# Kernel optimization log

Measured on AMD Instinct MI355X. Metric: run time of the kernel, lower is better.

Reference implementation:

```python
import jax, jax.numpy as jnp
import numpy as np

EMBED_DIM = 1024
NUM_HEADS = 16
HEAD_DIM = EMBED_DIM // NUM_HEADS


def setup_inputs() -> dict:
    key = jax.random.key(0)
    ks = jax.random.split(key, 9)
    B, N, D = 2, 2048, EMBED_DIM
    s = 1.0 / np.sqrt(D)
    inp = {
        "x": jax.random.normal(ks[0], (B, N, D), dtype=jnp.float32),
        "Wq": jax.random.uniform(ks[1], (D, D), jnp.float32, -s, s),
        "bq": jnp.zeros((D,), jnp.float32),
        "Wk": jax.random.uniform(ks[2], (D, D), jnp.float32, -s, s),
        "bk": jnp.zeros((D,), jnp.float32),
        "Wv": jax.random.uniform(ks[3], (D, D), jnp.float32, -s, s),
        "bv": jnp.zeros((D,), jnp.float32),
        "Wo": jax.random.uniform(ks[4], (D, D), jnp.float32, -s, s),
        "bo": jnp.zeros((D,), jnp.float32),
        "is_causal": 0,
    }
    return inp


def reference(x, Wq, bq, Wk, bk, Wv, bv, Wo, bo, is_causal):
    B, N, D = x.shape
    H, Hd = NUM_HEADS, HEAD_DIM
    # projections -> (B, H, N, Hd)
    def proj(W, b):
        return (x @ W.T + b).reshape(B, N, H, Hd).transpose(0, 2, 1, 3)
    q = proj(Wq, bq)
    k = proj(Wk, bk)
    v = proj(Wv, bv)
    # scaled dot-product attention with full (B,H,N,N) scores
    dots = jnp.einsum("bhqd,bhkd->bhqk", q, k) / np.sqrt(Hd).astype(np.float32)
    if is_causal:
        mask = jnp.tril(jnp.ones((N, N), dtype=bool))
        dots = jnp.where(mask, dots, -jnp.inf)
    attn = jax.nn.softmax(dots, axis=-1)
    out = jnp.einsum("bhqk,bhkd->bhqd", attn, v)  # (B,H,N,Hd)
    out = out.transpose(0, 2, 1, 3).reshape(B, N, D)
    return out @ Wo.T + bo
```

## Files before the change

### kernel.cpp

```cpp
#include <hip/hip_runtime.h>
#include <hip/hip_bf16.h>
#include <cstdint>
#include <cstddef>

#define DEVI __device__ __forceinline__

typedef __attribute__((ext_vector_type(8))) __bf16 bf16x8;
typedef __attribute__((ext_vector_type(4))) float  f32x4;
typedef __attribute__((ext_vector_type(4))) unsigned int uint4v;
typedef __attribute__((ext_vector_type(2))) unsigned int uint2v;

static constexpr int D_EMB = 1024;
static constexpr int NH    = 16;
static constexpr int HDIM  = 64;
static constexpr int BATCH = 2;
static constexpr int SEQ   = 2048;
static constexpr int MTOK  = BATCH * SEQ;
static constexpr int NQKV  = 3 * D_EMB;
static constexpr float L2E = 1.44269504088896340736f;
static constexpr float CSCALE = 0.125f * L2E;

#if __has_builtin(__builtin_amdgcn_exp2f)
#define EXP2F(x) __builtin_amdgcn_exp2f(x)
#else
#define EXP2F(x) exp2f(x)
#endif

typedef __attribute__((address_space(1))) unsigned int* gas_u32;
typedef __attribute__((address_space(3))) unsigned int* las_u32;

DEVI void gl_lds16(const void* g, void* l) {
  __builtin_amdgcn_global_load_lds((gas_u32)(void*)g, (las_u32)l, 16, 0, 0);
}

DEVI unsigned pack2bf(float lo, float hi) {
  unsigned short a = __builtin_bit_cast(unsigned short, (__bf16)lo);
  unsigned short b = __builtin_bit_cast(unsigned short, (__bf16)hi);
  return (unsigned)a | ((unsigned)b << 16);
}

__global__ __launch_bounds__(256) void cast_kernel(const float* __restrict__ in,
                                                   __bf16* __restrict__ out, int n8) {
  int i = blockIdx.x * 256 + threadIdx.x;
  if (i >= n8) return;
  const f32x4* p = (const f32x4*)(in + (size_t)i * 8);
  f32x4 a = p[0], b = p[1];
  bf16x8 o;
  o[0] = (__bf16)a[0]; o[1] = (__bf16)a[1]; o[2] = (__bf16)a[2]; o[3] = (__bf16)a[3];
  o[4] = (__bf16)b[0]; o[5] = (__bf16)b[1]; o[6] = (__bf16)b[2]; o[7] = (__bf16)b[3];
  *(bf16x8*)(out + (size_t)i * 8) = o;
}

__global__ __launch_bounds__(256) void cast_w4(const float* __restrict__ Wq,
                                               const float* __restrict__ Wk,
                                               const float* __restrict__ Wv,
                                               const float* __restrict__ Wo,
                                               __bf16* __restrict__ Wcat,
                                               __bf16* __restrict__ Wob) {
  const int which = blockIdx.y;
  const float* src = which == 0 ? Wq : which == 1 ? Wk : which == 2 ? Wv : Wo;
  __bf16* dst = which < 3 ? Wcat + (size_t)which * D_EMB * D_EMB : Wob;
  int i = blockIdx.x * 256 + threadIdx.x;
  const f32x4* p = (const f32x4*)(src + (size_t)i * 8);
  f32x4 a = p[0], b = p[1];
  bf16x8 o;
  o[0] = (__bf16)a[0]; o[1] = (__bf16)a[1]; o[2] = (__bf16)a[2]; o[3] = (__bf16)a[3];
  o[4] = (__bf16)b[0]; o[5] = (__bf16)b[1]; o[6] = (__bf16)b[2]; o[7] = (__bf16)b[3];
  *(bf16x8*)(dst + (size_t)i * 8) = o;
}

__global__ __launch_bounds__(512, 1) void gemm_qkv(const __bf16* __restrict__ A,
                                                   const __bf16* __restrict__ Bw,
                                                   const float* __restrict__ b0,
                                                   const float* __restrict__ b1,
                                                   const float* __restrict__ b2,
                                                   __bf16* __restrict__ C,
                                                   __bf16* __restrict__ Vt) {
  constexpr int lda = D_EMB, ldb = D_EMB, ldc = NQKV;
  constexpr int NT = D_EMB / 64;
  __shared__ __align__(16) unsigned char lds[131072];
  const int t = threadIdx.x;
  const int lane = t & 63, w = t >> 6;
  const int c = lane & 15, g = lane >> 4;
  const int wr = w >> 2, wc = w & 3;

  int fid = blockIdx.y * 12 + blockIdx.x;
  fid = (fid & 7) * 24 + (fid >> 3);
  const int bx = fid % 12, by = fid / 12;
  const int brow = by * 256, bcol = bx * 256;

  f32x4 acc[8][4] = {};

  int srow[2], schk[2];
#pragma unroll
  for (int i = 0; i < 2; i++) {
    int lb = i * 8192 + t * 16;
    int row = lb >> 7, ch = (lb & 127) >> 4;
    srow[i] = row; schk[i] = ch ^ (row & 7);
  }

  int offk[2];
#pragma unroll
  for (int kk = 0; kk < 2; kk++) offk[kk] = (((kk * 4 + g) ^ (c & 7)) << 4);
  int rowA[8], rowB[4];
#pragma unroll
  for (int m = 0; m < 8; m++) rowA[m] = (wr * 128 + m * 16 + c) * 128;
#pragma unroll
  for (int n = 0; n < 4; n++) rowB[n] = (wc * 64 + n * 16 + c) * 128;

#define STG_HALF(p, TN, NOFS)                                                       \
  do {                                                                              \
    if ((p) < 2) {                                                                  \
      _Pragma("unroll")                                                             \
      for (int i = 0; i < 2; i++)                                                   \
        gl_lds16(A + (size_t)(brow + (p) * 128 + srow[i]) * lda + (TN) * 64 + schk[i] * 8, \
                 lds + (NOFS) + (p) * 16384 + i * 8192 + t * 16);                   \
    } else {                                                                        \
      _Pragma("unroll")                                                             \
      for (int i = 0; i < 2; i++)                                                   \
        gl_lds16(Bw + (size_t)(bcol + ((p) & 1) * 128 + srow[i]) * ldb + (TN) * 64 + schk[i] * 8, \
                 lds + (NOFS) + 32768 + ((p) & 1) * 16384 + i * 8192 + t * 16);     \
    }                                                                               \
  } while (0)

#define PHASE(p, BOFS, NOFS, TN1, DO_STG)                                           \
  do {                                                                              \
    bf16x8 af[2][2];                                                                \
    if ((p) == 0) {                                                                 \
      _Pragma("unroll")                                                             \
      for (int n = 0; n < 4; n++)                                                   \
        _Pragma("unroll")                                                           \
        for (int kk = 0; kk < 2; kk++)                                              \
          bfr[n][kk] = *(const bf16x8*)(lds + (BOFS) + 32768 + rowB[n] + offk[kk]); \
    }                                                                               \
    _Pragma("unroll")                                                               \
    for (int mm = 0; mm < 2; mm++)                                                  \
      _Pragma("unroll")                                                             \
      for (int kk = 0; kk < 2; kk++)                                                \
        af[mm][kk] = *(const bf16x8*)(lds + (BOFS) + rowA[(p) * 2 + mm] + offk[kk]); \
    if (DO_STG) STG_HALF(p, TN1, NOFS);                                             \
    __builtin_amdgcn_s_barrier();                                                   \
    __builtin_amdgcn_s_setprio(1);                                                  \
    _Pragma("unroll")                                                               \
    for (int mm = 0; mm < 2; mm++)                                                  \
      _Pragma("unroll")                                                             \
      for (int n = 0; n < 4; n++)                                                   \
        _Pragma("unroll")                                                           \
        for (int kk = 0; kk < 2; kk++)                                              \
          acc[(p) * 2 + mm][n] = __builtin_amdgcn_mfma_f32_16x16x32_bf16(           \
              af[mm][kk], bfr[n][kk], acc[(p) * 2 + mm][n], 0, 0, 0);               \
    __builtin_amdgcn_s_setprio(0);                                                  \
    if ((p) == 3) asm volatile("s_waitcnt vmcnt(0)" ::: "memory");                  \
    __builtin_amdgcn_s_barrier();                                                   \
  } while (0)

#pragma unroll
  for (int p = 0; p < 4; p++) STG_HALF(p, 0, 0);
  __syncthreads();

  for (int tt = 0; tt < NT; tt += 2) {
    {
      bf16x8 bfr[4][2];
      const bool ds = (tt + 1 < NT);
      PHASE(0, 0, 65536, tt + 1, ds);
      PHASE(1, 0, 65536, tt + 1, ds);
      PHASE(2, 0, 65536, tt + 1, ds);
      PHASE(3, 0, 65536, tt + 1, ds);
    }
    {
      bf16x8 bfr[4][2];
      const bool ds = (tt + 2 < NT);
      PHASE(0, 65536, 0, tt + 2, ds);
      PHASE(1, 65536, 0, tt + 2, ds);
      PHASE(2, 65536, 0, tt + 2, ds);
      PHASE(3, 65536, 0, tt + 2, ds);
    }
  }
#undef STG_HALF
#undef PHASE

#pragma unroll
  for (int n = 0; n < 4; n++) {
    int col = bcol + wc * 64 + n * 16 + c;
    const float* bp = col < 1024 ? b0 : (col < 2048 ? b1 : b2);
    float bv = bp[col & 1023];
    float sc = col < 1024 ? CSCALE : 1.0f;
#pragma unroll
    for (int m = 0; m < 8; m++) {
      int row0 = brow + wr * 128 + m * 16 + g * 4;
      float v0 = (acc[m][n][0] + bv) * sc;
      float v1 = (acc[m][n][1] + bv) * sc;
      float v2 = (acc[m][n][2] + bv) * sc;
      float v3 = (acc[m][n][3] + bv) * sc;
      if (col >= 2048) {
        int cv = col - 2048;
        int h = cv >> 6, d = cv & 63;
        int bq = row0 >> 11;
        size_t vaddr = ((size_t)((bq * NH + h) * HDIM + d)) * SEQ + (row0 & (SEQ - 1));
        uint2v uu;
        uu[0] = pack2bf(v0, v1);
        uu[1] = pack2bf(v2, v3);
        *(uint2v*)(Vt + vaddr) = uu;
      } else {
        C[(size_t)(row0 + 0) * ldc + col] = (__bf16)v0;
        C[(size_t)(row0 + 1) * ldc + col] = (__bf16)v1;
        C[(size_t)(row0 + 2) * ldc + col] = (__bf16)v2;
        C[(size_t)(row0 + 3) * ldc + col] = (__bf16)v3;
      }
    }
  }
}

template <typename OutT, int BM>
__global__ __launch_bounds__(256) void gemm_bt(const __bf16* __restrict__ A,
                                               const __bf16* __restrict__ B,
                                               const float* __restrict__ b0,
                                               OutT* __restrict__ C,
                                               int K, int lda, int ldb, int ldc) {
  constexpr int ACH = BM / 32;
  constexpr int MR  = BM / 32;
  __shared__ __align__(16) unsigned char lds[BM * 128 + 16384];
  unsigned char* As = lds;
  unsigned char* Bs = lds + BM * 128;
  const int t = threadIdx.x;
  const int lane = t & 63;
  const int w = t >> 6;
  const int c = lane & 15, g = lane >> 4;
  const int wr = w >> 1, wc = w & 1;
  const int brow = blockIdx.y * BM;
  const int bcol = blockIdx.x * 128;

  f32x4 acc[MR][4] = {};

  int rs[4], chs[4];
#pragma unroll
  for (int i = 0; i < 4; i++) {
    int lb = i * 4096 + t * 16;
    int row = lb >> 7, ch = (lb & 127) >> 4;
    rs[i] = row; chs[i] = ch ^ (row & 7);
  }

  for (int k0 = 0; k0 < K; k0 += 64) {
#pragma unroll
    for (int i = 0; i < ACH; i++)
      gl_lds16(A + (size_t)(brow + rs[i]) * lda + k0 + chs[i] * 8,
               As + i * 4096 + t * 16);
#pragma unroll
    for (int i = 0; i < 4; i++)
      gl_lds16(B + (size_t)(bcol + rs[i]) * ldb + k0 + chs[i] * 8,
               Bs + i * 4096 + t * 16);
    __syncthreads();
#pragma unroll
    for (int kk = 0; kk < 2; kk++) {
      bf16x8 af[MR], bfr[4];
#pragma unroll
      for (int m = 0; m < MR; m++) {
        int row = wr * (BM / 2) + m * 16 + c;
        int ch = (kk * 4 + g) ^ (row & 7);
        af[m] = *(const bf16x8*)(As + row * 128 + ch * 16);
      }
#pragma unroll
      for (int n = 0; n < 4; n++) {
        int row = wc * 64 + n * 16 + c;
        int ch = (kk * 4 + g) ^ (row & 7);
        bfr[n] = *(const bf16x8*)(Bs + row * 128 + ch * 16);
      }
      __builtin_amdgcn_s_setprio(1);
#pragma unroll
      for (int m = 0; m < MR; m++)
#pragma unroll
        for (int n = 0; n < 4; n++)
          acc[m][n] = __builtin_amdgcn_mfma_f32_16x16x32_bf16(af[m], bfr[n], acc[m][n], 0, 0, 0);
      __builtin_amdgcn_s_setprio(0);
    }
    __syncthreads();
  }

#pragma unroll
  for (int n = 0; n < 4; n++) {
    int col = bcol + wc * 64 + n * 16 + c;
    float bv = b0[col];
#pragma unroll
    for (int m = 0; m < MR; m++) {
      int row0 = brow + wr * (BM / 2) + m * 16 + g * 4;
#pragma unroll
      for (int r = 0; r < 4; r++) {
        float v = acc[m][n][r] + bv;
        C[(size_t)(row0 + r) * ldc + col] = (OutT)v;
      }
    }
  }
}

__global__ __launch_bounds__(256, 2) void attn_fwd(const __bf16* __restrict__ Q,
                                                   const __bf16* __restrict__ Kg,
                                                   const __bf16* __restrict__ Vt,
                                                   __bf16* __restrict__ AO,
                                                   const int* __restrict__ causal_p) {
  __shared__ __align__(16) unsigned char lds[65536];
  const int t = threadIdx.x;
  const int lane = t & 63;
  const int w = t >> 6;
  const int c = lane & 15, g = lane >> 4;
  const int qhalf = w >> 1, parity = w & 1;
  const int bh = blockIdx.y;
  const int b = bh >> 4, h = bh & 15;
  const int q0 = blockIdx.x * 128;
  const int causal = causal_p[0];
  const int qbase = q0 + qhalf * 64;

  bf16x8 qf[4][2];
#pragma unroll
  for (int u = 0; u < 4; u++)
#pragma unroll
    for (int kk = 0; kk < 2; kk++)
      qf[u][kk] = *(const bf16x8*)(Q + (size_t)(b * SEQ + qbase + u * 16 + c) * NQKV +
                                   h * HDIM + kk * 32 + g * 8);

  f32x4 oacc[4][4] = {};
  float lrun[4] = {0.f, 0.f, 0.f, 0.f};

  int srow[2], schk[2];
#pragma unroll
  for (int i = 0; i < 2; i++) {
    int lb = i * 4096 + t * 16;
    int row = lb >> 7, ch = (lb & 127) >> 4;
    int sig = (row & 3) | ((row & 8) >> 1);
    srow[i] = row; schk[i] = ch ^ sig;
  }

  int voffK[8], voffV[8];
#pragma unroll
  for (int n = 0; n < 4; n++) {
    int row = ((n >> 1) << 5) + ((c >> 2) << 3) + ((n & 1) << 2) + (c & 3);
    int sig = (row & 3) | ((row & 8) >> 1);
#pragma unroll
    for (int kk = 0; kk < 2; kk++)
      voffK[n * 2 + kk] = parity * 16384 + row * 128 + (((kk * 4 + g) ^ sig) << 4);
  }
#pragma unroll
  for (int dt = 0; dt < 4; dt++) {
    int row = dt * 16 + c;
    int sig = (row & 3) | ((row & 8) >> 1);
#pragma unroll
    for (int kk2 = 0; kk2 < 2; kk2++)
      voffV[dt * 2 + kk2] = parity * 16384 + 8192 + row * 128 + (((kk2 * 4 + g) ^ sig) << 4);
  }

  const __bf16* Kbase = Kg + (size_t)b * SEQ * NQKV + h * HDIM;
  const __bf16* Vbase = Vt + (size_t)bh * HDIM * SEQ;

  const int kvend = causal ? (q0 + 128 < SEQ ? q0 + 128 : SEQ) : SEQ;
  const int npair = kvend >> 7;

#define STAGE_PAIR(JP, PB)                                                          \
  do {                                                                              \
    int kvn = (JP) << 7;                                                            \
    _Pragma("unroll")                                                               \
    for (int i = 0; i < 2; i++) {                                                   \
      gl_lds16(Kbase + (size_t)(kvn + srow[i]) * NQKV + schk[i] * 8,                \
               lds + (PB) + i * 4096 + t * 16);                                     \
      gl_lds16(Vbase + (size_t)srow[i] * SEQ + kvn + schk[i] * 8,                   \
               lds + (PB) + 8192 + i * 4096 + t * 16);                              \
      gl_lds16(Kbase + (size_t)(kvn + 64 + srow[i]) * NQKV + schk[i] * 8,           \
               lds + (PB) + 16384 + i * 4096 + t * 16);                             \
      gl_lds16(Vbase + (size_t)srow[i] * SEQ + kvn + 64 + schk[i] * 8,              \
               lds + (PB) + 24576 + i * 4096 + t * 16);                             \
    }                                                                               \
  } while (0)

#define ATTN_STEP(JV, BOFS, PBNEXT)                                                 \
  do {                                                                              \
    if ((JV) + 1 < npair) STAGE_PAIR((JV) + 1, PBNEXT);                             \
    f32x4 st[4][4] = {};                                                            \
    __builtin_amdgcn_s_setprio(1);                                                  \
    _Pragma("unroll")                                                               \
    for (int n = 0; n < 4; n++) {                                                   \
      _Pragma("unroll")                                                             \
      for (int kk = 0; kk < 2; kk++) {                                              \
        bf16x8 kf = *(const bf16x8*)(lds + (BOFS) + voffK[n * 2 + kk]);             \
        st[0][n] = __builtin_amdgcn_mfma_f32_16x16x32_bf16(kf, qf[0][kk], st[0][n], 0, 0, 0); \
        st[1][n] = __builtin_amdgcn_mfma_f32_16x16x32_bf16(kf, qf[1][kk], st[1][n], 0, 0, 0); \
        st[2][n] = __builtin_amdgcn_mfma_f32_16x16x32_bf16(kf, qf[2][kk], st[2][n], 0, 0, 0); \
        st[3][n] = __builtin_amdgcn_mfma_f32_16x16x32_bf16(kf, qf[3][kk], st[3][n], 0, 0, 0); \
      }                                                                             \
    }                                                                               \
    __builtin_amdgcn_s_setprio(0);                                                  \
    if (causal) {                                                                   \
      const int kv0 = ((JV) << 7) + parity * 64;                                    \
      _Pragma("unroll")                                                             \
      for (int u = 0; u < 4; u++) {                                                 \
        const int qrow_u = qbase + u * 16 + c;                                      \
        _Pragma("unroll")                                                           \
        for (int n = 0; n < 4; n++) {                                               \
          _Pragma("unroll")                                                         \
          for (int r = 0; r < 4; r++) {                                             \
            int kabs = kv0 + ((n >> 1) << 5) + (g << 3) + ((n & 1) << 2) + r;       \
            if (kabs > qrow_u) st[u][n][r] = -3.0e38f;                              \
          }                                                                         \
        }                                                                           \
      }                                                                             \
    }                                                                               \
    bf16x8 pfrag[4][2];                                                             \
    _Pragma("unroll")                                                               \
    for (int u = 0; u < 4; u++) {                                                   \
      _Pragma("unroll")                                                             \
      for (int n = 0; n < 4; n++) {                                                 \
        st[u][n][0] = EXP2F(st[u][n][0]);                                           \
        st[u][n][1] = EXP2F(st[u][n][1]);                                           \
        st[u][n][2] = EXP2F(st[u][n][2]);                                           \
        st[u][n][3] = EXP2F(st[u][n][3]);                                           \
      }                                                                             \
      float ps0 = (st[u][0][0] + st[u][0][1]) + (st[u][0][2] + st[u][0][3]);        \
      float ps1 = (st[u][1][0] + st[u][1][1]) + (st[u][1][2] + st[u][1][3]);        \
      float ps2 = (st[u][2][0] + st[u][2][1]) + (st[u][2][2] + st[u][2][3]);        \
      float ps3 = (st[u][3][0] + st[u][3][1]) + (st[u][3][2] + st[u][3][3]);        \
      lrun[u] += (ps0 + ps1) + (ps2 + ps3);                                         \
      _Pragma("unroll")                                                             \
      for (int kk2 = 0; kk2 < 2; kk2++) {                                           \
        int n0i = 2 * kk2, n1i = 2 * kk2 + 1;                                       \
        uint4v uu;                                                                  \
        uu[0] = pack2bf(st[u][n0i][0], st[u][n0i][1]);                              \
        uu[1] = pack2bf(st[u][n0i][2], st[u][n0i][3]);                              \
        uu[2] = pack2bf(st[u][n1i][0], st[u][n1i][1]);                              \
        uu[3] = pack2bf(st[u][n1i][2], st[u][n1i][3]);                              \
        pfrag[u][kk2] = __builtin_bit_cast(bf16x8, uu);                             \
      }                                                                             \
    }                                                                               \
    __builtin_amdgcn_s_setprio(1);                                                  \
    _Pragma("unroll")                                                               \
    for (int dt = 0; dt < 4; dt++) {                                                \
      _Pragma("unroll")                                                             \
      for (int kk2 = 0; kk2 < 2; kk2++) {                                           \
        bf16x8 vf = *(const bf16x8*)(lds + (BOFS) + voffV[dt * 2 + kk2]);           \
        oacc[0][dt] = __builtin_amdgcn_mfma_f32_16x16x32_bf16(vf, pfrag[0][kk2], oacc[0][dt], 0, 0, 0); \
        oacc[1][dt] = __builtin_amdgcn_mfma_f32_16x16x32_bf16(vf, pfrag[1][kk2], oacc[1][dt], 0, 0, 0); \
        oacc[2][dt] = __builtin_amdgcn_mfma_f32_16x16x32_bf16(vf, pfrag[2][kk2], oacc[2][dt], 0, 0, 0); \
        oacc[3][dt] = __builtin_amdgcn_mfma_f32_16x16x32_bf16(vf, pfrag[3][kk2], oacc[3][dt], 0, 0, 0); \
      }                                                                             \
    }                                                                               \
    __builtin_amdgcn_s_setprio(0);                                                  \
    __syncthreads();                                                                \
  } while (0)

  STAGE_PAIR(0, 0);
  __syncthreads();

  for (int j = 0; j < npair; j += 2) {
    ATTN_STEP(j, 0, 32768);
    if (j + 1 < npair) ATTN_STEP(j + 1, 32768, 0);
  }

  const int mbase = qhalf * 16640;
  float* mf = (float*)(lds + mbase);
  float* ml = (float*)(lds + mbase + 16384);
  if (parity == 1) {
#pragma unroll
    for (int u = 0; u < 4; u++) {
#pragma unroll
      for (int dt = 0; dt < 4; dt++) {
#pragma unroll
        for (int r = 0; r < 4; r++) {
          int d = dt * 16 + 4 * g + r;
          mf[(d << 6) + u * 16 + c] = oacc[u][dt][r];
        }
      }
      float l = lrun[u];
      l += __shfl_xor(l, 16);
      l += __shfl_xor(l, 32);
      ml[u * 16 + c] = l;
    }
  }
  __syncthreads();
  if (parity == 0) {
#pragma unroll
    for (int u = 0; u < 4; u++) {
      float l = lrun[u];
      l += __shfl_xor(l, 16);
      l += __shfl_xor(l, 32);
      l += ml[u * 16 + c];
      float inv = 1.0f / l;
      const int qrow_u = qbase + u * 16 + c;
#pragma unroll
      for (int dt = 0; dt < 4; dt++) {
        f32x4 o;
#pragma unroll
        for (int r = 0; r < 4; r++) {
          int d = dt * 16 + 4 * g + r;
          o[r] = (oacc[u][dt][r] + mf[(d << 6) + u * 16 + c]) * inv;
        }
        uint2v uu;
        uu[0] = pack2bf(o[0], o[1]);
        uu[1] = pack2bf(o[2], o[3]);
        *(uint2v*)(AO + (size_t)(b * SEQ + qrow_u) * NQKV + h * HDIM + dt * 16 + g * 4) = uu;
      }
    }
  }
#undef STAGE_PAIR
#undef ATTN_STEP
}

extern "C" void kernel_launch(void* const* d_in, const int* in_sizes, int n_in,
                              void* d_out, int out_size, void* d_ws, size_t ws_size,
                              hipStream_t stream) {
  const float* x  = (const float*)d_in[0];
  const float* Wq = (const float*)d_in[1];
  const float* bq = (const float*)d_in[2];
  const float* Wk = (const float*)d_in[3];
  const float* bk = (const float*)d_in[4];
  const float* Wv = (const float*)d_in[5];
  const float* bv = (const float*)d_in[6];
  const float* Wo = (const float*)d_in[7];
  const float* bo = (const float*)d_in[8];
  const int* causal = (const int*)d_in[9];
  float* out = (float*)d_out;

  char* ws = (char*)d_ws;
  const size_t SZ_TOK = (size_t)MTOK * D_EMB * sizeof(__bf16);
  const size_t SZ_W   = (size_t)D_EMB * D_EMB * sizeof(__bf16);
  __bf16* xb   = (__bf16*)(ws);
  __bf16* Wob  = (__bf16*)(ws + SZ_TOK);
  __bf16* Wcat = (__bf16*)(ws + SZ_TOK + SZ_W);
  __bf16* QKV  = (__bf16*)(ws + SZ_TOK + 4 * SZ_W);
  __bf16* Vtb  = (__bf16*)(ws + 4 * SZ_TOK + 4 * SZ_W);
  __bf16* Qb   = QKV;
  __bf16* Kb   = QKV + D_EMB;
  __bf16* AOb  = QKV + 2 * D_EMB;

  cast_kernel<<<MTOK * D_EMB / 2048, 256, 0, stream>>>(x, xb, MTOK * D_EMB / 8);
  cast_w4<<<dim3(D_EMB * D_EMB / 2048, 4), 256, 0, stream>>>(Wq, Wk, Wv, Wo, Wcat, Wob);

  gemm_qkv<<<dim3(NQKV / 256, MTOK / 256), 512, 0, stream>>>(
      xb, Wcat, bq, bk, bv, QKV, Vtb);

  attn_fwd<<<dim3(SEQ / 128, BATCH * NH), 256, 0, stream>>>(Qb, Kb, Vtb, AOb, causal);

  gemm_bt<float, 64><<<dim3(D_EMB / 128, MTOK / 64), 256, 0, stream>>>(
      AOb, Wob, bo, out, D_EMB, NQKV, D_EMB, D_EMB);
}
```

Baseline: 114.9 us.

## Merge cast kernels and restructure QKV GEMM warp tiling with finer vmcnt pipelining

Replaces the two fp32-to-bf16 cast launches with a single kernel that dispatches on block index, removing one launch. In the QKV GEMM, each wave now covers all 256 rows and a 32-column strip instead of a 128x64 tile. The per-half staging order becomes A0, B0, B1, A1 and uses partial vmcnt waits instead of a full drain each tile, so loads overlap more with MFMA work. The changed wave tiling loads more A fragments per wave from LDS, which raises LDS read traffic, and the hand-counted vmcnt values must stay correct.

```diff
diff --git a/kernel.cpp b/kernel.cpp
--- a/kernel.cpp
+++ b/kernel.cpp
@@ -39,34 +39,30 @@
   return (unsigned)a | ((unsigned)b << 16);
 }
 
-__global__ __launch_bounds__(256) void cast_kernel(const float* __restrict__ in,
-                                                   __bf16* __restrict__ out, int n8) {
-  int i = blockIdx.x * 256 + threadIdx.x;
-  if (i >= n8) return;
-  const f32x4* p = (const f32x4*)(in + (size_t)i * 8);
+__global__ __launch_bounds__(256) void cast_all(const float* __restrict__ x,
+                                                const float* __restrict__ Wq,
+                                                const float* __restrict__ Wk,
+                                                const float* __restrict__ Wv,
+                                                const float* __restrict__ Wo,
+                                                __bf16* __restrict__ xb,
+                                                __bf16* __restrict__ Wcat,
+                                                __bf16* __restrict__ Wob) {
+  const int bid = blockIdx.x;
+  const float* src;
+  __bf16* dst;
+  size_t off;
+  if (bid < 2048)      { src = x;  dst = xb;   off = (size_t)bid * 2048; }
+  else if (bid < 2560) { src = Wq; dst = Wcat; off = (size_t)(bid - 2048) * 2048; }
+  else if (bid < 3072) { src = Wk; dst = Wcat + (1u << 20); off = (size_t)(bid - 2560) * 2048; }
+  else if (bid < 3584) { src = Wv; dst = Wcat + (2u << 20); off = (size_t)(bid - 3072) * 2048; }
+  else                 { src = Wo; dst = Wob;  off = (size_t)(bid - 3584) * 2048; }
+  size_t i = off + (size_t)threadIdx.x * 8;
+  const f32x4* p = (const f32x4*)(src + i);
   f32x4 a = p[0], b = p[1];
   bf16x8 o;
   o[0] = (__bf16)a[0]; o[1] = (__bf16)a[1]; o[2] = (__bf16)a[2]; o[3] = (__bf16)a[3];
   o[4] = (__bf16)b[0]; o[5] = (__bf16)b[1]; o[6] = (__bf16)b[2]; o[7] = (__bf16)b[3];
-  *(bf16x8*)(out + (size_t)i * 8) = o;
-}
-
-__global__ __launch_bounds__(256) void cast_w4(const float* __restrict__ Wq,
-                                               const float* __restrict__ Wk,
-                                               const float* __restrict__ Wv,
-                                               const float* __restrict__ Wo,
-                                               __bf16* __restrict__ Wcat,
-                                               __bf16* __restrict__ Wob) {
-  const int which = blockIdx.y;
-  const float* src = which == 0 ? Wq : which == 1 ? Wk : which == 2 ? Wv : Wo;
-  __bf16* dst = which < 3 ? Wcat + (size_t)which * D_EMB * D_EMB : Wob;
-  int i = blockIdx.x * 256 + threadIdx.x;
-  const f32x4* p = (const f32x4*)(src + (size_t)i * 8);
-  f32x4 a = p[0], b = p[1];
-  bf16x8 o;
-  o[0] = (__bf16)a[0]; o[1] = (__bf16)a[1]; o[2] = (__bf16)a[2]; o[3] = (__bf16)a[3];
-  o[4] = (__bf16)b[0]; o[5] = (__bf16)b[1]; o[6] = (__bf16)b[2]; o[7] = (__bf16)b[3];
-  *(bf16x8*)(dst + (size_t)i * 8) = o;
+  *(bf16x8*)(dst + i) = o;
 }
 
 __global__ __launch_bounds__(512, 1) void gemm_qkv(const __bf16* __restrict__ A,
@@ -82,14 +78,13 @@
   const int t = threadIdx.x;
   const int lane = t & 63, w = t >> 6;
   const int c = lane & 15, g = lane >> 4;
-  const int wr = w >> 2, wc = w & 3;
 
   int fid = blockIdx.y * 12 + blockIdx.x;
   fid = (fid & 7) * 24 + (fid >> 3);
   const int bx = fid % 12, by = fid / 12;
   const int brow = by * 256, bcol = bx * 256;
 
-  f32x4 acc[8][4] = {};
+  f32x4 acc[16][2] = {};
 
   int srow[2], schk[2];
 #pragma unroll
@@ -102,92 +97,121 @@
   int offk[2];
 #pragma unroll
   for (int kk = 0; kk < 2; kk++) offk[kk] = (((kk * 4 + g) ^ (c & 7)) << 4);
-  int rowA[8], rowB[4];
-#pragma unroll
-  for (int m = 0; m < 8; m++) rowA[m] = (wr * 128 + m * 16 + c) * 128;
-#pragma unroll
-  for (int n = 0; n < 4; n++) rowB[n] = (wc * 64 + n * 16 + c) * 128;
-
-#define STG_HALF(p, TN, NOFS)                                                       \
+  int rowA[16], rowB[2];
+#pragma unroll
+  for (int m = 0; m < 16; m++) {
+    int r = m * 16 + c;
+    rowA[m] = (r >> 7) * 16384 + (r & 127) * 128;
+  }
+#pragma unroll
+  for (int n = 0; n < 2; n++) {
+    int r = w * 32 + n * 16 + c;
+    rowB[n] = 32768 + (r >> 7) * 16384 + (r & 127) * 128;
+  }
+
+#define STG_A(H, TN, NOFS)                                                          \
   do {                                                                              \
-    if ((p) < 2) {                                                                  \
-      _Pragma("unroll")                                                             \
-      for (int i = 0; i < 2; i++)                                                   \
-        gl_lds16(A + (size_t)(brow + (p) * 128 + srow[i]) * lda + (TN) * 64 + schk[i] * 8, \
-                 lds + (NOFS) + (p) * 16384 + i * 8192 + t * 16);                   \
-    } else {                                                                        \
-      _Pragma("unroll")                                                             \
-      for (int i = 0; i < 2; i++)                                                   \
-        gl_lds16(Bw + (size_t)(bcol + ((p) & 1) * 128 + srow[i]) * ldb + (TN) * 64 + schk[i] * 8, \
-                 lds + (NOFS) + 32768 + ((p) & 1) * 16384 + i * 8192 + t * 16);     \
-    }                                                                               \
+    _Pragma("unroll")                                                               \
+    for (int i = 0; i < 2; i++)                                                     \
+      gl_lds16(A + (size_t)(brow + (H) * 128 + srow[i]) * lda + (TN) * 64 + schk[i] * 8, \
+               lds + (NOFS) + (H) * 16384 + i * 8192 + t * 16);                     \
   } while (0)
 
-#define PHASE(p, BOFS, NOFS, TN1, DO_STG)                                           \
+#define STG_B(H, TN, NOFS)                                                          \
   do {                                                                              \
-    bf16x8 af[2][2];                                                                \
-    if ((p) == 0) {                                                                 \
-      _Pragma("unroll")                                                             \
-      for (int n = 0; n < 4; n++)                                                   \
+    _Pragma("unroll")                                                               \
+    for (int i = 0; i < 2; i++)                                                     \
+      gl_lds16(Bw + (size_t)(bcol + (H) * 128 + srow[i]) * ldb + (TN) * 64 + schk[i] * 8, \
+               lds + (NOFS) + 32768 + (H) * 16384 + i * 8192 + t * 16);             \
+  } while (0)
+
+#define PHASE(p, BOFS, NOFS, TN1, DO_STG, LAST)                                     \
+  do {                                                                              \
+    bf16x8 af[4][2];                                                                \
+    if (p == 0) {                                                                   \
+      _Pragma("unroll")                                                             \
+      for (int n = 0; n < 2; n++)                                                   \
         _Pragma("unroll")                                                           \
         for (int kk = 0; kk < 2; kk++)                                              \
-          bfr[n][kk] = *(const bf16x8*)(lds + (BOFS) + 32768 + rowB[n] + offk[kk]); \
-    }                                                                               \
-    _Pragma("unroll")                                                               \
-    for (int mm = 0; mm < 2; mm++)                                                  \
+          bfr[n][kk] = *(const bf16x8*)(lds + (BOFS) + rowB[n] + offk[kk]);         \
+    }                                                                               \
+    _Pragma("unroll")                                                               \
+    for (int mm = 0; mm < 4; mm++)                                                  \
       _Pragma("unroll")                                                             \
       for (int kk = 0; kk < 2; kk++)                                                \
-        af[mm][kk] = *(const bf16x8*)(lds + (BOFS) + rowA[(p) * 2 + mm] + offk[kk]); \
-    if (DO_STG) STG_HALF(p, TN1, NOFS);                                             \
+        af[mm][kk] = *(const bf16x8*)(lds + (BOFS) + rowA[(p) * 4 + mm] + offk[kk]); \
+    if (DO_STG) {                                                                   \
+      if ((p) == 0) STG_A(0, TN1, NOFS);                                            \
+      else if ((p) == 1) STG_B(0, TN1, NOFS);                                       \
+      else if ((p) == 2) STG_B(1, TN1, NOFS);                                       \
+      else STG_A(1, TN1, NOFS);                                                     \
+    }                                                                               \
     __builtin_amdgcn_s_barrier();                                                   \
     __builtin_amdgcn_s_setprio(1);                                                  \
     _Pragma("unroll")                                                               \
-    for (int mm = 0; mm < 2; mm++)                                                  \
-      _Pragma("unroll")                                                             \
-      for (int n = 0; n < 4; n++)                                                   \
+    for (int mm = 0; mm < 4; mm++)                                                  \
+      _Pragma("unroll")                                                             \
+      for (int n = 0; n < 2; n++)                                                   \
         _Pragma("unroll")                                                           \
         for (int kk = 0; kk < 2; kk++)                                              \
-          acc[(p) * 2 + mm][n] = __builtin_amdgcn_mfma_f32_16x16x32_bf16(           \
-              af[mm][kk], bfr[n][kk], acc[(p) * 2 + mm][n], 0, 0, 0);               \
+          acc[(p) * 4 + mm][n] = __builtin_amdgcn_mfma_f32_16x16x32_bf16(           \
+              af[mm][kk], bfr[n][kk], acc[(p) * 4 + mm][n], 0, 0, 0);               \
     __builtin_amdgcn_s_setprio(0);                                                  \
-    if ((p) == 3) asm volatile("s_waitcnt vmcnt(0)" ::: "memory");                  \
+    if ((p) == 1) {                                                                 \
+      if (LAST) asm volatile("s_waitcnt vmcnt(0)" ::: "memory");                    \
+      else      asm volatile("s_waitcnt vmcnt(4)" ::: "memory");                    \
+    }                                                                               \
+    if ((p) == 3 && !(LAST)) asm volatile("s_waitcnt vmcnt(2)" ::: "memory");       \
     __builtin_amdgcn_s_barrier();                                                   \
   } while (0)
 
-#pragma unroll
-  for (int p = 0; p < 4; p++) STG_HALF(p, 0, 0);
-  __syncthreads();
-
-  for (int tt = 0; tt < NT; tt += 2) {
+  STG_A(0, 0, 0); STG_B(0, 0, 0); STG_B(1, 0, 0); STG_A(1, 0, 0);
+  asm volatile("s_waitcnt vmcnt(2)" ::: "memory");
+  __builtin_amdgcn_s_barrier();
+
+  for (int tt = 0; tt < NT - 2; tt += 2) {
     {
-      bf16x8 bfr[4][2];
-      const bool ds = (tt + 1 < NT);
-      PHASE(0, 0, 65536, tt + 1, ds);
-      PHASE(1, 0, 65536, tt + 1, ds);
-      PHASE(2, 0, 65536, tt + 1, ds);
-      PHASE(3, 0, 65536, tt + 1, ds);
+      bf16x8 bfr[2][2];
+      PHASE(0, 0, 65536, tt + 1, true, false);
+      PHASE(1, 0, 65536, tt + 1, true, false);
+      PHASE(2, 0, 65536, tt + 1, true, false);
+      PHASE(3, 0, 65536, tt + 1, true, false);
     }
     {
-      bf16x8 bfr[4][2];
-      const bool ds = (tt + 2 < NT);
-      PHASE(0, 65536, 0, tt + 2, ds);
-      PHASE(1, 65536, 0, tt + 2, ds);
-      PHASE(2, 65536, 0, tt + 2, ds);
-      PHASE(3, 65536, 0, tt + 2, ds);
-    }
-  }
-#undef STG_HALF
+      bf16x8 bfr[2][2];
+      PHASE(0, 65536, 0, tt + 2, true, false);
+      PHASE(1, 65536, 0, tt + 2, true, false);
+      PHASE(2, 65536, 0, tt + 2, true, false);
+      PHASE(3, 65536, 0, tt + 2, true, false);
+    }
+  }
+  {
+    bf16x8 bfr[2][2];
+    PHASE(0, 0, 65536, NT - 1, true, false);
+    PHASE(1, 0, 65536, NT - 1, true, false);
+    PHASE(2, 0, 65536, NT - 1, true, false);
+    PHASE(3, 0, 65536, NT - 1, true, false);
+  }
+  {
+    bf16x8 bfr[2][2];
+    PHASE(0, 65536, 0, 0, false, true);
+    PHASE(1, 65536, 0, 0, false, true);
+    PHASE(2, 65536, 0, 0, false, true);
+    PHASE(3, 65536, 0, 0, false, true);
+  }
+#undef STG_A
+#undef STG_B
 #undef PHASE
 
 #pragma unroll
-  for (int n = 0; n < 4; n++) {
-    int col = bcol + wc * 64 + n * 16 + c;
+  for (int n = 0; n < 2; n++) {
+    int col = bcol + w * 32 + n * 16 + c;
     const float* bp = col < 1024 ? b0 : (col < 2048 ? b1 : b2);
     float bv = bp[col & 1023];
     float sc = col < 1024 ? CSCALE : 1.0f;
 #pragma unroll
-    for (int m = 0; m < 8; m++) {
-      int row0 = brow + wr * 128 + m * 16 + g * 4;
+    for (int m = 0; m < 16; m++) {
+      int row0 = brow + m * 16 + g * 4;
       float v0 = (acc[m][n][0] + bv) * sc;
       float v1 = (acc[m][n][1] + bv) * sc;
       float v2 = (acc[m][n][2] + bv) * sc;
@@ -527,8 +551,7 @@
   __bf16* Kb   = QKV + D_EMB;
   __bf16* AOb  = QKV + 2 * D_EMB;
 
-  cast_kernel<<<MTOK * D_EMB / 2048, 256, 0, stream>>>(x, xb, MTOK * D_EMB / 8);
-  cast_w4<<<dim3(D_EMB * D_EMB / 2048, 4), 256, 0, stream>>>(Wq, Wk, Wv, Wo, Wcat, Wob);
+  cast_all<<<4096, 256, 0, stream>>>(x, Wq, Wk, Wv, Wo, xb, Wcat, Wob);
 
   gemm_qkv<<<dim3(NQKV / 256, MTOK / 256), 512, 0, stream>>>(
       xb, Wcat, bq, bk, bv, QKV, Vtb);
```

New measurement: 115.6 us. Within noise of the previous version (+0.6%).
